# Optimization experiments

Hardware: AMD Instinct MI355X
Metric: run time of the kernel (lower is better)

Reference implementation:

```python
import jax, jax.numpy as jnp
import numpy as np

TEMPERATURE = 8.0  # init_kwargs temperature
NEG_INF = -1e16


def setup_inputs() -> dict:
    key = jax.random.key(0)
    ks = jax.random.split(key, 8)
    B, S, D = 4, 1024, 64
    q = jax.random.normal(ks[0], (B, S, D), dtype=jnp.float32)
    k = jax.random.normal(ks[1], (B, S, D), dtype=jnp.float32)
    v = jax.random.normal(ks[2], (B, S, D), dtype=jnp.float32)
    # MLP params (Linear(2D,50) -> ReLU -> Linear(50,25) -> ReLU -> Linear(25,1))
    W1 = jax.random.normal(ks[3], (2 * D, 50), dtype=jnp.float32) * (1.0 / np.sqrt(2 * D))
    b1 = jnp.zeros((50,), dtype=jnp.float32)
    W2 = jax.random.normal(ks[4], (50, 25), dtype=jnp.float32) * (1.0 / np.sqrt(50))
    b2 = jnp.zeros((25,), dtype=jnp.float32)
    W3 = jax.random.normal(ks[5], (25, 1), dtype=jnp.float32) * (1.0 / np.sqrt(25))
    b3 = jnp.zeros((1,), dtype=jnp.float32)
    # causal mask: True where attention is disallowed (j > i)
    mask = jnp.triu(jnp.ones((S, S), dtype=bool), k=1)
    mask = jnp.broadcast_to(mask, (B, S, S))
    return {"q": q, "k": k, "v": v, "W1": W1, "b1": b1, "W2": W2,
            "b2": b2, "W3": W3, "b3": b3, "mask": mask}


def reference(q, k, v, W1, b1, W2, b2, W3, b3, mask):
    D = q.shape[-1]
    # cat([q_i, k_j]) @ W1 == q_i @ W1[:D] + k_j @ W1[D:]; avoids the
    # explicit [B,S,S,2D] concat the torch code materializes.
    Wq, Wk = W1[:D], W1[D:]
    hq = jnp.einsum('bsd,df->bsf', q, Wq)           # [B,S,50]
    hk = jnp.einsum('btd,df->btf', k, Wk)           # [B,S,50]
    h1 = jax.nn.relu(hq[:, :, None, :] + hk[:, None, :, :] + b1)  # [B,S,S,50]
    h2 = jax.nn.relu(jnp.einsum('bstf,fg->bstg', h1, W2) + b2)    # [B,S,S,25]
    scores = (jnp.einsum('bstg,go->bsto', h2, W3) + b3)[..., 0]    # [B,S,S]
    scores = scores / TEMPERATURE
    scores = jnp.where(mask, NEG_INF, scores)
    attn = jax.nn.softmax(scores, axis=2)           # softmax over key dim
    out = jnp.einsum('bst,btd->bsd', attn, v)       # [B,S,D]
    return (out, attn)
```

## Files before the change

kernel.cpp:

```cpp
#include <hip/hip_runtime.h>
#include <hip/hip_fp16.h>
#include <math.h>

#define BB 4
#define SQL 1024
#define DD 64
#define NFP 64
#define TEMP_INV 0.125f

typedef __attribute__((ext_vector_type(8))) _Float16 f16x8;
typedef __attribute__((ext_vector_type(4))) float f32x4;

__global__ __launch_bounds__(256) void proj_kernel(
    const float* __restrict__ q, const float* __restrict__ k,
    const float* __restrict__ W1, const float* __restrict__ b1,
    _Float16* __restrict__ hq, _Float16* __restrict__ hk)
{
  const int lane = threadIdx.x & 63;
  const int wave = threadIdx.x >> 6;
  const int unit = blockIdx.x * 4 + wave;
  const int isK  = unit >> 12;
  const int row  = unit & 4095;
  __shared__ float r[4][DD];
  const float* src = isK ? k : q;
  r[wave][lane] = src[row * DD + lane];
  __syncthreads();
  float acc0 = 0.f, acc1 = 0.f;
  if (lane < 50) {
    acc0 = isK ? 0.f : b1[lane];
    const float* w = W1 + isK * DD * 50 + lane;
#pragma unroll
    for (int d = 0; d < DD; d += 2) {
      acc0 = fmaf(r[wave][d],     w[d * 50],       acc0);
      acc1 = fmaf(r[wave][d + 1], w[(d + 1) * 50], acc1);
    }
  }
  _Float16* dst = isK ? hk : hq;
  dst[row * NFP + lane] = (_Float16)(acc0 + acc1);
}

__global__ __launch_bounds__(512, 4) void score_kernel(
    const _Float16* __restrict__ hq, const _Float16* __restrict__ hk,
    const float* __restrict__ W2, const float* __restrict__ b2,
    const float* __restrict__ W3, const float* __restrict__ b3,
    float* __restrict__ sc_g)
{
  const int bid  = blockIdx.x;
  const int half = blockIdx.y;
  const int b    = blockIdx.z;
  const int tid  = threadIdx.x;
  const int lane = tid & 63;
  const int wave = tid >> 6;
  const int lo   = lane & 15;
  const int grp  = lane >> 4;

  __shared__ _Float16 shq[8][NFP];

  const int sA = 4 * bid;
  const int sB = 1020 - 4 * bid;

  if (tid < 64) {
    int r = tid >> 3, c8 = (tid & 7) * 8;
    int s = (r < 4) ? (sA + r) : (sB + r - 4);
    *(float4*)(&shq[r][c8]) =
        *(const float4*)(hq + ((size_t)(b * SQL + s)) * NFP + c8);
  }

  f16x8 w2f[2][2];
#pragma unroll
  for (int gt = 0; gt < 2; ++gt) {
    int g = lo + 16 * gt;
#pragma unroll
    for (int c = 0; c < 2; ++c) {
      f16x8 fr;
#pragma unroll
      for (int j = 0; j < 8; ++j) {
        int f = c * 32 + grp * 8 + j;
        float val = (f < 50 && g < 25) ? W2[f * 25 + g] : 0.f;
        fr[j] = (_Float16)val;
      }
      w2f[gt][c] = fr;
    }
  }
  float w3a[4], w3b[4], b2a[4], b2b[4];
#pragma unroll
  for (int rr = 0; rr < 4; ++rr) {
    int g0 = grp * 4 + rr;
    int g1 = 16 + grp * 4 + rr;
    w3a[rr] = W3[g0];
    b2a[rr] = b2[g0];
    w3b[rr] = (g1 < 25) ? W3[g1] : 0.f;
    b2b[rr] = (g1 < 25) ? b2[g1] : 0.f;
  }
  const float b3v = b3[0];

  __syncthreads();

  const int ntiles = ((sB + 3) >> 5) + 1;
  const _Float16* hkb = hk + (size_t)b * SQL * NFP;

  for (int tt = wave + (half << 3); tt < ntiles; tt += 16) {
    const int tbase = tt << 5;
    f16x8 hkv[2][2];
#pragma unroll
    for (int th = 0; th < 2; ++th) {
      const _Float16* p = hkb + (size_t)(tbase + th * 16 + lo) * NFP + grp * 8;
#pragma unroll
      for (int c = 0; c < 2; ++c)
        hkv[th][c] = *(const f16x8*)(p + c * 32);
    }
#pragma unroll 1
    for (int pr = 0; pr < 4; ++pr) {
      const int s_h = sB + pr;
      if (s_h < tbase) continue;
      const int s_l = sA + pr;
      const bool has_l = (s_l >= tbase);

      f16x8 hqh[2], hql[2];
#pragma unroll
      for (int c = 0; c < 2; ++c)
        hqh[c] = *(const f16x8*)(&shq[pr + 4][c * 32 + grp * 8]);
      if (has_l) {
#pragma unroll
        for (int c = 0; c < 2; ++c)
          hql[c] = *(const f16x8*)(&shq[pr][c * 32 + grp * 8]);
      }

      f32x4 acch[2][2] = {{{0.f,0.f,0.f,0.f},{0.f,0.f,0.f,0.f}},
                          {{0.f,0.f,0.f,0.f},{0.f,0.f,0.f,0.f}}};
      f32x4 accl[2][2] = {{{0.f,0.f,0.f,0.f},{0.f,0.f,0.f,0.f}},
                          {{0.f,0.f,0.f,0.f},{0.f,0.f,0.f,0.f}}};
#pragma unroll
      for (int th = 0; th < 2; ++th) {
#pragma unroll
        for (int c = 0; c < 2; ++c) {
          f16x8 bh = __builtin_elementwise_max(hqh[c] + hkv[th][c], (f16x8)0);
          acch[th][0] = __builtin_amdgcn_mfma_f32_16x16x32_f16(w2f[0][c], bh, acch[th][0], 0, 0, 0);
          acch[th][1] = __builtin_amdgcn_mfma_f32_16x16x32_f16(w2f[1][c], bh, acch[th][1], 0, 0, 0);
          if (has_l) {
            f16x8 bl = __builtin_elementwise_max(hql[c] + hkv[th][c], (f16x8)0);
            accl[th][0] = __builtin_amdgcn_mfma_f32_16x16x32_f16(w2f[0][c], bl, accl[th][0], 0, 0, 0);
            accl[th][1] = __builtin_amdgcn_mfma_f32_16x16x32_f16(w2f[1][c], bl, accl[th][1], 0, 0, 0);
          }
        }
      }
      float sh[2], sl[2];
#pragma unroll
      for (int th = 0; th < 2; ++th) {
        float part = 0.f;
#pragma unroll
        for (int rr = 0; rr < 4; ++rr) {
          part += fmaxf(acch[th][0][rr] + b2a[rr], 0.f) * w3a[rr];
          part += fmaxf(acch[th][1][rr] + b2b[rr], 0.f) * w3b[rr];
        }
        part += __shfl_xor(part, 16);
        part += __shfl_xor(part, 32);
        sh[th] = (part + b3v) * TEMP_INV;
      }
      if (lane < 32)
        sc_g[((size_t)(b * SQL + s_h) << 10) + tbase + lane] = (lane & 16) ? sh[1] : sh[0];
      if (has_l) {
#pragma unroll
        for (int th = 0; th < 2; ++th) {
          float part = 0.f;
#pragma unroll
          for (int rr = 0; rr < 4; ++rr) {
            part += fmaxf(accl[th][0][rr] + b2a[rr], 0.f) * w3a[rr];
            part += fmaxf(accl[th][1][rr] + b2b[rr], 0.f) * w3b[rr];
          }
          part += __shfl_xor(part, 16);
          part += __shfl_xor(part, 32);
          sl[th] = (part + b3v) * TEMP_INV;
        }
        if (lane < 32)
          sc_g[((size_t)(b * SQL + s_l) << 10) + tbase + lane] = (lane & 16) ? sl[1] : sl[0];
      }
    }
  }
}

__global__ __launch_bounds__(256) void smpv_kernel(
    const float* __restrict__ sc_g, const float* __restrict__ v,
    float* __restrict__ out, float* __restrict__ attn)
{
  const int s    = blockIdx.x;
  const int b    = blockIdx.y;
  const int tid  = threadIdx.x;
  const int lane = tid & 63;
  const int wave = tid >> 6;

  __shared__ float sp[SQL];
  __shared__ float red[2][4];
  __shared__ float outred[4][DD];

  const float* srow = sc_g + ((size_t)(b * SQL + s) << 10);

  float vv[4];
  float m = -INFINITY;
#pragma unroll
  for (int c = 0; c < 4; ++c) {
    int t = tid + c * 256;
    vv[c] = (t <= s) ? srow[t] : -INFINITY;
    m = fmaxf(m, vv[c]);
  }
#pragma unroll
  for (int off = 32; off; off >>= 1) m = fmaxf(m, __shfl_xor(m, off));
  if (lane == 0) red[0][wave] = m;
  __syncthreads();
  m = fmaxf(fmaxf(red[0][0], red[0][1]), fmaxf(red[0][2], red[0][3]));

  float sum = 0.f;
#pragma unroll
  for (int c = 0; c < 4; ++c) {
    float e = (tid + c * 256 <= s) ? __expf(vv[c] - m) : 0.f;
    vv[c] = e;
    sum += e;
  }
#pragma unroll
  for (int off = 32; off; off >>= 1) sum += __shfl_xor(sum, off);
  if (lane == 0) red[1][wave] = sum;
  __syncthreads();
  sum = red[1][0] + red[1][1] + red[1][2] + red[1][3];
  const float inv = 1.f / sum;

  float* arow = attn + ((size_t)(b * SQL + s)) * SQL;
#pragma unroll
  for (int c = 0; c < 4; ++c) {
    float a = vv[c] * inv;
    arow[tid + c * 256] = a;
    sp[tid + c * 256] = a;
  }
  __syncthreads();

  const int cs = ((((s + 1) + 3) >> 2) + 3) & ~3;
  const int t0 = wave * cs;
  const int te = min((wave + 1) * cs, SQL);
  const float* vb = v + (size_t)(b * SQL) * DD + lane;
  float a0 = 0.f, a1 = 0.f, a2 = 0.f, a3 = 0.f;
  for (int t = t0; t < te; t += 4) {
    float4 av = *(const float4*)(&sp[t]);
    a0 = fmaf(av.x, vb[(size_t)(t)     * DD], a0);
    a1 = fmaf(av.y, vb[(size_t)(t + 1) * DD], a1);
    a2 = fmaf(av.z, vb[(size_t)(t + 2) * DD], a2);
    a3 = fmaf(av.w, vb[(size_t)(t + 3) * DD], a3);
  }
  outred[wave][lane] = (a0 + a1) + (a2 + a3);
  __syncthreads();
  if (tid < DD)
    out[((size_t)(b * SQL + s)) * DD + tid] =
        outred[0][tid] + outred[1][tid] + outred[2][tid] + outred[3][tid];
}

extern "C" void kernel_launch(void* const* d_in, const int* in_sizes, int n_in,
                              void* d_out, int out_size, void* d_ws, size_t ws_size,
                              hipStream_t stream) {
  const float* q  = (const float*)d_in[0];
  const float* k  = (const float*)d_in[1];
  const float* v  = (const float*)d_in[2];
  const float* W1 = (const float*)d_in[3];
  const float* b1 = (const float*)d_in[4];
  const float* W2 = (const float*)d_in[5];
  const float* b2 = (const float*)d_in[6];
  const float* W3 = (const float*)d_in[7];
  const float* b3 = (const float*)d_in[8];

  float* out  = (float*)d_out;
  float* attn = out + BB * SQL * DD;

  float* sc_g = (float*)d_ws;
  _Float16* hq = (_Float16*)(sc_g + (size_t)BB * SQL * SQL);
  _Float16* hk = hq + BB * SQL * NFP;

  proj_kernel<<<dim3(2048), 256, 0, stream>>>(q, k, W1, b1, hq, hk);
  score_kernel<<<dim3(128, 2, BB), 512, 0, stream>>>(hq, hk, W2, b2, W3, b3, sc_g);
  smpv_kernel<<<dim3(SQL, BB), 256, 0, stream>>>(sc_g, v, out, attn);
}
```

Before: 155.9 us.

## Process eight query rows per softmax-PV block with balanced causal pairing

Each block of the softmax/PV kernel now handles eight rows, four from the start and four mirrored from the end of the sequence, so causal work is balanced across blocks. Each wave does a per-row softmax with wave-level reductions only, and stores the probabilities as fp16 in a transposed shared buffer. Every V element loaded is then reused across eight rows instead of one, which cuts global V traffic. The cost is fp16 rounding of the probabilities in the PV product, more registers per thread, and far fewer blocks (512 instead of 4096).

New measurement: 164.3 us. +5.4%, slower.

```diff
diff --git a/kernel.cpp b/kernel.cpp
--- a/kernel.cpp
+++ b/kernel.cpp
@@ -183,72 +183,82 @@
     const float* __restrict__ sc_g, const float* __restrict__ v,
     float* __restrict__ out, float* __restrict__ attn)
 {
-  const int s    = blockIdx.x;
+  const int bid  = blockIdx.x;
   const int b    = blockIdx.y;
   const int tid  = threadIdx.x;
   const int lane = tid & 63;
   const int wave = tid >> 6;
 
-  __shared__ float sp[SQL];
-  __shared__ float red[2][4];
-  __shared__ float outred[4][DD];
-
-  const float* srow = sc_g + ((size_t)(b * SQL + s) << 10);
-
-  float vv[4];
-  float m = -INFINITY;
-#pragma unroll
-  for (int c = 0; c < 4; ++c) {
-    int t = tid + c * 256;
-    vv[c] = (t <= s) ? srow[t] : -INFINITY;
-    m = fmaxf(m, vv[c]);
-  }
-#pragma unroll
-  for (int off = 32; off; off >>= 1) m = fmaxf(m, __shfl_xor(m, off));
-  if (lane == 0) red[0][wave] = m;
-  __syncthreads();
-  m = fmaxf(fmaxf(red[0][0], red[0][1]), fmaxf(red[0][2], red[0][3]));
-
-  float sum = 0.f;
-#pragma unroll
-  for (int c = 0; c < 4; ++c) {
-    float e = (tid + c * 256 <= s) ? __expf(vv[c] - m) : 0.f;
-    vv[c] = e;
-    sum += e;
-  }
-#pragma unroll
-  for (int off = 32; off; off >>= 1) sum += __shfl_xor(sum, off);
-  if (lane == 0) red[1][wave] = sum;
-  __syncthreads();
-  sum = red[1][0] + red[1][1] + red[1][2] + red[1][3];
-  const float inv = 1.f / sum;
-
-  float* arow = attn + ((size_t)(b * SQL + s)) * SQL;
-#pragma unroll
-  for (int c = 0; c < 4; ++c) {
-    float a = vv[c] * inv;
-    arow[tid + c * 256] = a;
-    sp[tid + c * 256] = a;
-  }
-  __syncthreads();
-
-  const int cs = ((((s + 1) + 3) >> 2) + 3) & ~3;
+  __shared__ _Float16 spt[SQL][8];
+  __shared__ float outred[4][8][DD];
+
+  const int sA = 4 * bid;
+  const int sB = 1020 - 4 * bid;
+
+#pragma unroll
+  for (int rr = 0; rr < 2; ++rr) {
+    const int r = wave + rr * 4;
+    const int s = rr ? (sB + wave) : (sA + wave);
+    const float* srow = sc_g + ((size_t)(b * SQL + s) << 10);
+    float vv[16];
+    float m = -INFINITY;
+#pragma unroll
+    for (int c = 0; c < 16; ++c) {
+      int t = c * 64 + lane;
+      vv[c] = (t <= s) ? srow[t] : -INFINITY;
+      m = fmaxf(m, vv[c]);
+    }
+#pragma unroll
+    for (int off = 32; off; off >>= 1) m = fmaxf(m, __shfl_xor(m, off));
+    float sum = 0.f;
+#pragma unroll
+    for (int c = 0; c < 16; ++c) {
+      float e = (c * 64 + lane <= s) ? __expf(vv[c] - m) : 0.f;
+      vv[c] = e;
+      sum += e;
+    }
+#pragma unroll
+    for (int off = 32; off; off >>= 1) sum += __shfl_xor(sum, off);
+    const float inv = 1.f / sum;
+    float* arow = attn + ((size_t)(b * SQL + s)) * SQL;
+#pragma unroll
+    for (int c = 0; c < 16; ++c) {
+      float a = vv[c] * inv;
+      arow[c * 64 + lane] = a;
+      spt[c * 64 + lane][r] = (_Float16)a;
+    }
+  }
+  __syncthreads();
+
+  const int ntv = sB + 4;
+  const int cs = ((((ntv + 3) >> 2) + 1) & ~1);
   const int t0 = wave * cs;
-  const int te = min((wave + 1) * cs, SQL);
+  const int te = min(t0 + cs, SQL);
   const float* vb = v + (size_t)(b * SQL) * DD + lane;
-  float a0 = 0.f, a1 = 0.f, a2 = 0.f, a3 = 0.f;
-  for (int t = t0; t < te; t += 4) {
-    float4 av = *(const float4*)(&sp[t]);
-    a0 = fmaf(av.x, vb[(size_t)(t)     * DD], a0);
-    a1 = fmaf(av.y, vb[(size_t)(t + 1) * DD], a1);
-    a2 = fmaf(av.z, vb[(size_t)(t + 2) * DD], a2);
-    a3 = fmaf(av.w, vb[(size_t)(t + 3) * DD], a3);
-  }
-  outred[wave][lane] = (a0 + a1) + (a2 + a3);
-  __syncthreads();
-  if (tid < DD)
-    out[((size_t)(b * SQL + s)) * DD + tid] =
-        outred[0][tid] + outred[1][tid] + outred[2][tid] + outred[3][tid];
+  float acc[8] = {0.f, 0.f, 0.f, 0.f, 0.f, 0.f, 0.f, 0.f};
+  for (int t = t0; t < te; t += 2) {
+    f16x8 p0 = *(const f16x8*)(&spt[t][0]);
+    f16x8 p1 = *(const f16x8*)(&spt[t + 1][0]);
+    float v0 = vb[(size_t)t * DD];
+    float v1 = vb[(size_t)(t + 1) * DD];
+#pragma unroll
+    for (int r = 0; r < 8; ++r) {
+      acc[r] = fmaf((float)p0[r], v0, acc[r]);
+      acc[r] = fmaf((float)p1[r], v1, acc[r]);
+    }
+  }
+#pragma unroll
+  for (int r = 0; r < 8; ++r) outred[wave][r][lane] = acc[r];
+  __syncthreads();
+
+#pragma unroll
+  for (int rr = 0; rr < 2; ++rr) {
+    const int r = wave + rr * 4;
+    const int s = rr ? (sB + wave) : (sA + wave);
+    float o = outred[0][r][lane] + outred[1][r][lane]
+            + outred[2][r][lane] + outred[3][r][lane];
+    out[((size_t)(b * SQL + s)) * DD + lane] = o;
+  }
 }
 
 extern "C" void kernel_launch(void* const* d_in, const int* in_sizes, int n_in,
@@ -273,5 +283,5 @@
 
   proj_kernel<<<dim3(2048), 256, 0, stream>>>(q, k, W1, b1, hq, hk);
   score_kernel<<<dim3(128, 2, BB), 512, 0, stream>>>(hq, hk, W2, b2, W3, b3, sc_g);
-  smpv_kernel<<<dim3(SQL, BB), 256, 0, stream>>>(sc_g, v, out, attn);
-}
+  smpv_kernel<<<dim3(128, BB), 256, 0, stream>>>(sc_g, v, out, attn);
+}
```
